# Kernel tuning notes

Measured on AMD Instinct MI355X. Metric: run time of the kernel, lower is better.

Reference implementation:

```python
import jax, jax.numpy as jnp
import numpy as np
import math

B, S, C = 4, 2048, 128
H, DK, DV, K = 8, 64, 64, 3


def setup_inputs() -> dict:
    key = jax.random.key(0)
    ks = jax.random.split(key, 12)
    sd = 0.05
    return {
        "x": jax.random.normal(ks[0], (B, S, C), dtype=jnp.float32),
        "length": jax.random.randint(ks[1], (B,), 1, S + 1, dtype=jnp.int32),
        "wq": jax.random.normal(ks[2], (H * DK, C, K), dtype=jnp.float32) * sd,
        "bq": jnp.zeros((H * DK,), dtype=jnp.float32),
        "wk": jax.random.normal(ks[3], (H * DK, C, K), dtype=jnp.float32) * sd,
        "bk": jnp.zeros((H * DK,), dtype=jnp.float32),
        "wv": jax.random.normal(ks[4], (H * DV, C), dtype=jnp.float32) * sd,
        "bv": jnp.zeros((H * DV,), dtype=jnp.float32),
        "w1": jax.random.normal(ks[5], (DV, H * DV), dtype=jnp.float32) * sd,
        "b1": jnp.zeros((DV,), dtype=jnp.float32),
        "w2": jax.random.normal(ks[6], (1, DV), dtype=jnp.float32) * sd,
        "b2": jnp.zeros((1,), dtype=jnp.float32),
    }


def _causal_conv(x, w, b):
    # x: (b,s,c), w: (o,c,k) torch Conv1d layout -> (b,s,o), causal (left) padding
    y = jax.lax.conv_general_dilated(
        x.transpose(0, 2, 1), w, window_strides=(1,), padding=[(K - 1, 0)],
        dimension_numbers=("NCH", "OIH", "NCH"))
    return y.transpose(0, 2, 1) + b


def _split_heads(x, d):
    b, s, _ = x.shape
    return x.reshape(b, s, H, d).transpose(0, 2, 1, 3)  # (b,h,s,d)


def reference(x, length, wq, bq, wk, bk, wv, bv, w1, b1, w2, b2):
    q = _split_heads(_causal_conv(x, wq, bq), DK)            # (b,h,s,dk)
    k = _split_heads(_causal_conv(x, wk, bk), DK)            # (b,h,s,dk)
    v = _split_heads(jax.nn.relu(x @ wv.T + bv), DV)         # (b,h,s,dv)

    attn = jnp.einsum("bhqd,bhkd->bhqk", q, k) / math.sqrt(DK)
    # future mask: additive -1e9 above the diagonal (matches triu * -1e9 + softmax)
    future = jnp.triu(jnp.ones((S, S), dtype=attn.dtype), k=1) * (-1e9)
    score = jax.nn.softmax(attn + future, axis=-1)
    # padding mask: zero query rows >= length[b]
    row_valid = (jnp.arange(S)[None, :] < length[:, None]).astype(score.dtype)
    score = score * row_valid[:, None, :, None]              # (b,h,s,s)

    out1 = jnp.einsum("bhqk,bhkd->bhqd", score, v)           # (b,h,s,dv)
    out2 = out1.transpose(0, 2, 1, 3).reshape(x.shape[0], S, H * DV)
    out3 = jax.nn.relu(out2 @ w1.T + b1) @ w2.T + b2         # (b,s,1)
    return out3, score
```

## Files before the change

kernel.cpp:

```cpp
#include <hip/hip_runtime.h>

#define S_ 2048
#define C_ 128
#define B_ 4
#define H_ 8
#define D_ 64

typedef __attribute__((ext_vector_type(8))) short bf16x8;
typedef __attribute__((ext_vector_type(4))) float f32x4;

__device__ inline unsigned short f2bf(float f) {
    union { float f; unsigned int u; } c; c.f = f;
    unsigned int u = c.u;
    unsigned int r = (u + 0x7FFFu + ((u >> 16) & 1u)) >> 16;
    return (unsigned short)r;
}
__device__ inline float bf2f(unsigned short s) {
    union { unsigned int u; float f; } c; c.u = ((unsigned int)s) << 16;
    return c.f;
}

__global__ __launch_bounds__(256) void prep_kernel(
    const float* __restrict__ x,
    const float* __restrict__ wq, const float* __restrict__ wk,
    const float* __restrict__ wv, const float* __restrict__ w1,
    unsigned short* __restrict__ xh,
    unsigned short* __restrict__ wPackQ, unsigned short* __restrict__ wPackK,
    unsigned short* __restrict__ wPackV, float* __restrict__ w1T)
{
    int idx = blockIdx.x * 256 + threadIdx.x;
    if (idx < 1048576) {
        xh[idx] = f2bf(x[idx]);
    } else if (idx < 1245184) {
        int i = idx - 1048576;
        int t = i >> 16, r = i & 65535;
        int o = r >> 7, c = r & 127;
        wPackQ[i] = f2bf(wq[o * 384 + c * 3 + t]);
    } else if (idx < 1441792) {
        int i = idx - 1245184;
        int t = i >> 16, r = i & 65535;
        int o = r >> 7, c = r & 127;
        wPackK[i] = f2bf(wk[o * 384 + c * 3 + t]);
    } else if (idx < 1507328) {
        int i = idx - 1441792;
        wPackV[i] = f2bf(wv[i]);
    } else if (idx < 1540096) {
        int i = idx - 1507328;
        int j = i >> 6, d = i & 63;
        w1T[i] = w1[d * 512 + j];
    }
}

__global__ __launch_bounds__(256) void qkv_kernel(
    const unsigned short* __restrict__ xh,
    const unsigned short* __restrict__ wPackQ, const unsigned short* __restrict__ wPackK,
    const unsigned short* __restrict__ wPackV,
    const float* __restrict__ bq, const float* __restrict__ bk,
    const float* __restrict__ bv,
    unsigned short* __restrict__ Qh, unsigned short* __restrict__ Kh,
    unsigned short* __restrict__ VhT)
{
    __shared__ __align__(16) short xs[130 * 136];
    __shared__ __align__(16) short ws[64 * 136];

    int s0 = blockIdx.x * 128;
    int h = blockIdx.y;
    int b = blockIdx.z;
    int bh = b * H_ + h;
    int tid = threadIdx.x;
    int w = tid >> 6;
    int lane = tid & 63;
    int col = lane & 15;
    int quad = lane >> 4;

    for (int i = tid; i < 2080; i += 256) {
        int row = i >> 4, c8 = (i & 15) << 3;
        int s = s0 - 2 + row;
        uint4 v = {0u, 0u, 0u, 0u};
        if (s >= 0) v = *(const uint4*)&xh[((long)b * S_ + s) * C_ + c8];
        *(uint4*)&xs[row * 136 + c8] = v;
    }

    for (int sec = 0; sec < 3; sec++) {
        const unsigned short* wsel = (sec == 0) ? wPackQ : (sec == 1) ? wPackK : wPackV;
        int tlo = (sec == 2) ? 2 : 0;

        f32x4 acc[2][4];
        #pragma unroll
        for (int rt = 0; rt < 2; rt++)
            #pragma unroll
            for (int nt = 0; nt < 4; nt++) acc[rt][nt] = (f32x4){0.f, 0.f, 0.f, 0.f};

        for (int t = tlo; t < 3; t++) {
            if (!(sec == 0 && t == 0)) __syncthreads();
            long wbase = (sec == 2) ? ((long)h * 8192)
                                    : ((long)t * 65536 + (long)h * 8192);
            for (int i = tid; i < 1024; i += 256) {
                int row = i >> 4, c8 = (i & 15) << 3;
                *(uint4*)&ws[row * 136 + c8] = *(const uint4*)&wsel[wbase + row * 128 + c8];
            }
            __syncthreads();

            #pragma unroll
            for (int kc = 0; kc < 4; kc++) {
                int ko = kc * 32 + quad * 8;
                bf16x8 a0 = *(const bf16x8*)&xs[(w * 32 + col + t) * 136 + ko];
                bf16x8 a1 = *(const bf16x8*)&xs[(w * 32 + 16 + col + t) * 136 + ko];
                #pragma unroll
                for (int nt = 0; nt < 4; nt++) {
                    bf16x8 bfr = *(const bf16x8*)&ws[(nt * 16 + col) * 136 + ko];
                    acc[0][nt] = __builtin_amdgcn_mfma_f32_16x16x32_bf16(a0, bfr, acc[0][nt], 0, 0, 0);
                    acc[1][nt] = __builtin_amdgcn_mfma_f32_16x16x32_bf16(a1, bfr, acc[1][nt], 0, 0, 0);
                }
            }
        }

        if (sec == 0) {
            #pragma unroll
            for (int nt = 0; nt < 4; nt++) {
                float bias = bq[h * 64 + nt * 16 + col];
                #pragma unroll
                for (int rt = 0; rt < 2; rt++)
                    #pragma unroll
                    for (int r = 0; r < 4; r++) {
                        int s = s0 + w * 32 + rt * 16 + quad * 4 + r;
                        Qh[((long)bh * S_ + s) * D_ + nt * 16 + col] =
                            f2bf((acc[rt][nt][r] + bias) * 0.18033688011112042f);
                    }
            }
        } else if (sec == 1) {
            #pragma unroll
            for (int nt = 0; nt < 4; nt++) {
                float bias = bk[h * 64 + nt * 16 + col];
                #pragma unroll
                for (int rt = 0; rt < 2; rt++)
                    #pragma unroll
                    for (int r = 0; r < 4; r++) {
                        int s = s0 + w * 32 + rt * 16 + quad * 4 + r;
                        Kh[((long)bh * S_ + s) * D_ + nt * 16 + col] =
                            f2bf(acc[rt][nt][r] + bias);
                    }
            }
        } else {
            __syncthreads();
            #pragma unroll
            for (int nt = 0; nt < 4; nt++) {
                float bias = bv[h * 64 + nt * 16 + col];
                #pragma unroll
                for (int rt = 0; rt < 2; rt++)
                    #pragma unroll
                    for (int r = 0; r < 4; r++) {
                        int sl = w * 32 + rt * 16 + quad * 4 + r;
                        ws[(nt * 16 + col) * 136 + sl] =
                            (short)f2bf(fmaxf(acc[rt][nt][r] + bias, 0.f));
                    }
            }
            __syncthreads();
            for (int i = tid; i < 1024; i += 256) {
                int row = i >> 4, c8 = (i & 15) << 3;
                *(uint4*)&VhT[((long)bh * D_ + row) * S_ + s0 + c8] =
                    *(const uint4*)&ws[row * 136 + c8];
            }
        }
    }
}

#define PST 78
__global__ __launch_bounds__(256) void attn_kernel(
    const unsigned short* __restrict__ Qh, const unsigned short* __restrict__ Kh,
    const unsigned short* __restrict__ VhT, const int* __restrict__ length,
    float* __restrict__ score, float* __restrict__ out2)
{
    __shared__ __align__(16) short Pfh[64 * PST];

    int idx = blockIdx.x;
    int xcd = idx & 7;
    int slot = idx >> 3;
    int t = slot >> 2;
    int qt = (t < 16) ? t : 47 - t;
    int bh = xcd * 4 + (slot & 3);
    int b = bh >> 3, h = bh & 7;
    int q0 = qt * 64;
    int tid = threadIdx.x;
    int w = tid >> 6;
    int lane = tid & 63;
    int col = lane & 15;
    int quad = lane >> 4;
    int len = length[b];

    const unsigned short* Qb = Qh + (long)bh * S_ * D_;
    const unsigned short* Kb = Kh + (long)bh * S_ * D_;
    const unsigned short* Vtb = VhT + (long)bh * D_ * S_;
    float* scb = score + (long)bh * S_ * S_;

    int arow = w * 16 + col;
    bf16x8 aq0 = *(const bf16x8*)&Qb[(q0 + arow) * D_ + quad * 8];
    bf16x8 aq1 = *(const bf16x8*)&Qb[(q0 + arow) * D_ + 32 + quad * 8];

    float lrun[4];
    #pragma unroll
    for (int r = 0; r < 4; r++) lrun[r] = 0.f;

    for (int kt = 0; kt <= qt; kt++) {
        bf16x8 kf0[4], kf1[4];
        #pragma unroll
        for (int n = 0; n < 4; n++) {
            const unsigned short* kp = &Kb[(kt * 64 + n * 16 + col) * D_ + quad * 8];
            kf0[n] = *(const bf16x8*)kp;
            kf1[n] = *(const bf16x8*)(kp + 32);
        }
        f32x4 acc[4];
        #pragma unroll
        for (int n = 0; n < 4; n++) acc[n] = (f32x4){0.f, 0.f, 0.f, 0.f};
        #pragma unroll
        for (int n = 0; n < 4; n++) {
            acc[n] = __builtin_amdgcn_mfma_f32_16x16x32_bf16(aq0, kf0[n], acc[n], 0, 0, 0);
            acc[n] = __builtin_amdgcn_mfma_f32_16x16x32_bf16(aq1, kf1[n], acc[n], 0, 0, 0);
        }
        if (kt == qt) {
            #pragma unroll
            for (int n = 0; n < 4; n++) {
                int kk = kt * 64 + n * 16 + col;
                #pragma unroll
                for (int r = 0; r < 4; r++) {
                    int q = q0 + w * 16 + quad * 4 + r;
                    if (kk > q) acc[n][r] = -1.0e30f;
                }
            }
        }
        #pragma unroll
        for (int r = 0; r < 4; r++) {
            lrun[r] += exp2f(acc[0][r]) + exp2f(acc[1][r]) +
                       exp2f(acc[2][r]) + exp2f(acc[3][r]);
        }
    }

    #pragma unroll
    for (int off = 1; off < 16; off <<= 1) {
        #pragma unroll
        for (int r = 0; r < 4; r++) lrun[r] += __shfl_xor(lrun[r], off, 64);
    }
    float linv[4];
    #pragma unroll
    for (int r = 0; r < 4; r++) linv[r] = 1.0f / lrun[r];

    f32x4 oacc[4];
    #pragma unroll
    for (int n = 0; n < 4; n++) oacc[n] = (f32x4){0.f, 0.f, 0.f, 0.f};

    int prow = w * 16 + quad * 4;
    for (int kt = 0; kt <= qt; kt++) {
        bf16x8 kf0[4], kf1[4], vf0[4], vf1[4];
        #pragma unroll
        for (int n = 0; n < 4; n++) {
            const unsigned short* kp = &Kb[(kt * 64 + n * 16 + col) * D_ + quad * 8];
            kf0[n] = *(const bf16x8*)kp;
            kf1[n] = *(const bf16x8*)(kp + 32);
        }
        #pragma unroll
        for (int n = 0; n < 4; n++) {
            const unsigned short* vp = &Vtb[(n * 16 + col) * S_ + kt * 64 + quad * 8];
            vf0[n] = *(const bf16x8*)vp;
            vf1[n] = *(const bf16x8*)(vp + 32);
        }

        f32x4 acc[4];
        #pragma unroll
        for (int n = 0; n < 4; n++) acc[n] = (f32x4){0.f, 0.f, 0.f, 0.f};
        #pragma unroll
        for (int n = 0; n < 4; n++) {
            acc[n] = __builtin_amdgcn_mfma_f32_16x16x32_bf16(aq0, kf0[n], acc[n], 0, 0, 0);
            acc[n] = __builtin_amdgcn_mfma_f32_16x16x32_bf16(aq1, kf1[n], acc[n], 0, 0, 0);
        }

        bool diag = (kt == qt);
        #pragma unroll
        for (int n = 0; n < 4; n++) {
            int kk = kt * 64 + n * 16 + col;
            float p[4];
            #pragma unroll
            for (int r = 0; r < 4; r++) {
                int q = q0 + prow + r;
                float pv = exp2f(acc[n][r]) * linv[r];
                if (q >= len || (diag && kk > q)) pv = 0.f;
                p[r] = pv;
                __builtin_nontemporal_store(pv, &scb[(long)q * S_ + kk]);
            }
            unsigned int pk01, pk23;
            asm("v_cvt_pk_bf16_f32 %0, %1, %2" : "=v"(pk01) : "v"(p[0]), "v"(p[1]));
            asm("v_cvt_pk_bf16_f32 %0, %1, %2" : "=v"(pk23) : "v"(p[2]), "v"(p[3]));
            int pcol = n * 16 + col;
            Pfh[prow * PST + pcol]       = (short)(pk01 & 0xFFFFu);
            Pfh[(prow + 1) * PST + pcol] = (short)(pk01 >> 16);
            Pfh[(prow + 2) * PST + pcol] = (short)(pk23 & 0xFFFFu);
            Pfh[(prow + 3) * PST + pcol] = (short)(pk23 >> 16);
        }

        bf16x8 pa0 = *(const bf16x8*)&Pfh[(w * 16 + col) * PST + quad * 8];
        bf16x8 pa1 = *(const bf16x8*)&Pfh[(w * 16 + col) * PST + 32 + quad * 8];
        #pragma unroll
        for (int n = 0; n < 4; n++) {
            oacc[n] = __builtin_amdgcn_mfma_f32_16x16x32_bf16(pa0, vf0[n], oacc[n], 0, 0, 0);
            oacc[n] = __builtin_amdgcn_mfma_f32_16x16x32_bf16(pa1, vf1[n], oacc[n], 0, 0, 0);
        }
    }

    #pragma unroll
    for (int n = 0; n < 4; n++) {
        #pragma unroll
        for (int r = 0; r < 4; r++) {
            int q = q0 + w * 16 + quad * 4 + r;
            out2[((long)(b * S_ + q)) * 512 + h * 64 + n * 16 + col] = oacc[n][r];
        }
    }

    f32x4 z = (f32x4){0.f, 0.f, 0.f, 0.f};
    for (int kt2 = qt + 1; kt2 < 32; kt2++) {
        #pragma unroll
        for (int it = 0; it < 4; it++) {
            int idx2 = tid + it * 256;
            int rr = idx2 >> 4, cc = idx2 & 15;
            __builtin_nontemporal_store(z,
                (f32x4*)&scb[(long)(q0 + rr) * S_ + kt2 * 64 + cc * 4]);
        }
    }
}

__global__ __launch_bounds__(256) void mlp_kernel(
    const float* __restrict__ out2, const float* __restrict__ w1T,
    const float* __restrict__ b1, const float* __restrict__ w2,
    const float* __restrict__ b2, float* __restrict__ out3)
{
    __shared__ float xr[2048];
    int sg0 = blockIdx.x * 4;
    int tid = threadIdx.x;
    for (int i = tid; i < 2048; i += 256) xr[i] = out2[(long)sg0 * 512 + i];
    __syncthreads();

    int sl = tid >> 6, d = tid & 63;
    float acc = 0.f;
    const float* xp = &xr[sl * 512];
    #pragma unroll 8
    for (int j = 0; j < 512; j++) acc += xp[j] * w1T[j * 64 + d];
    float hval = fmaxf(acc + b1[d], 0.f);
    float p = hval * w2[d];
    #pragma unroll
    for (int off = 32; off > 0; off >>= 1) p += __shfl_xor(p, off, 64);
    if (d == 0) out3[sg0 + sl] = p + b2[0];
}

extern "C" void kernel_launch(void* const* d_in, const int* in_sizes, int n_in,
                              void* d_out, int out_size, void* d_ws, size_t ws_size,
                              hipStream_t stream) {
    const float* x      = (const float*)d_in[0];
    const int*   length = (const int*)  d_in[1];
    const float* wq     = (const float*)d_in[2];
    const float* bq     = (const float*)d_in[3];
    const float* wk     = (const float*)d_in[4];
    const float* bk     = (const float*)d_in[5];
    const float* wv     = (const float*)d_in[6];
    const float* bv     = (const float*)d_in[7];
    const float* w1     = (const float*)d_in[8];
    const float* b1     = (const float*)d_in[9];
    const float* w2     = (const float*)d_in[10];
    const float* b2     = (const float*)d_in[11];

    float* out3  = (float*)d_out;
    float* score = (float*)d_out + 8192;

    float* ws  = (float*)d_ws;
    unsigned short* xh     = (unsigned short*)ws;  ws += 524288;
    unsigned short* wPackQ = (unsigned short*)ws;  ws += 98304;
    unsigned short* wPackK = (unsigned short*)ws;  ws += 98304;
    unsigned short* wPackV = (unsigned short*)ws;  ws += 32768;
    float* w1T = ws;  ws += 32768;
    unsigned short* Qh  = (unsigned short*)ws;  ws += 2097152;
    unsigned short* Kh  = (unsigned short*)ws;  ws += 2097152;
    unsigned short* VhT = (unsigned short*)ws;  ws += 2097152;
    float* o2  = ws;  ws += 4194304;

    hipLaunchKernelGGL(prep_kernel, dim3(6016), dim3(256), 0, stream,
                       x, wq, wk, wv, w1, xh, wPackQ, wPackK, wPackV, w1T);
    hipLaunchKernelGGL(qkv_kernel, dim3(16, 8, 4), dim3(256), 0, stream,
                       xh, wPackQ, wPackK, wPackV, bq, bk, bv, Qh, Kh, VhT);
    hipLaunchKernelGGL(attn_kernel, dim3(1024), dim3(256), 0, stream,
                       Qh, Kh, VhT, length, score, o2);
    hipLaunchKernelGGL(mlp_kernel, dim3(2048), dim3(256), 0, stream,
                       o2, w1T, b1, w2, b2, out3);
}
```

Baseline: 759.1 us.

## Stage K/V tiles through double-buffered LDS and vectorize score stores

The attention kernel now stages K (and, in the second pass, transposed V) tiles into double-buffered shared memory with coalesced 16-byte loads. The next tile's loads are issued before the current tile's MFMA work, replacing per-lane scattered global fragment loads. Score writes go from scalar per-element stores to row-contiguous float4 nontemporal stores read back from the bf16 P tile. Because of that readback, stored scores are now bf16-rounded, which may affect accuracy. The prep and MLP kernels are also vectorized with float4 conversion and a repacked w1 layout, at the cost of extra barriers per tile.

```diff
diff --git a/kernel.cpp b/kernel.cpp
--- a/kernel.cpp
+++ b/kernel.cpp
@@ -26,28 +26,31 @@
     const float* __restrict__ wv, const float* __restrict__ w1,
     unsigned short* __restrict__ xh,
     unsigned short* __restrict__ wPackQ, unsigned short* __restrict__ wPackK,
-    unsigned short* __restrict__ wPackV, float* __restrict__ w1T)
+    unsigned short* __restrict__ wPackV, float* __restrict__ w1T4)
 {
     int idx = blockIdx.x * 256 + threadIdx.x;
-    if (idx < 1048576) {
-        xh[idx] = f2bf(x[idx]);
-    } else if (idx < 1245184) {
-        int i = idx - 1048576;
+    if (idx < 262144) {
+        float4 v = *(const float4*)&x[idx * 4];
+        ushort4 o;
+        o.x = f2bf(v.x); o.y = f2bf(v.y); o.z = f2bf(v.z); o.w = f2bf(v.w);
+        *(ushort4*)&xh[idx * 4] = o;
+    } else if (idx < 458752) {
+        int i = idx - 262144;
         int t = i >> 16, r = i & 65535;
         int o = r >> 7, c = r & 127;
         wPackQ[i] = f2bf(wq[o * 384 + c * 3 + t]);
-    } else if (idx < 1441792) {
-        int i = idx - 1245184;
+    } else if (idx < 655360) {
+        int i = idx - 458752;
         int t = i >> 16, r = i & 65535;
         int o = r >> 7, c = r & 127;
         wPackK[i] = f2bf(wk[o * 384 + c * 3 + t]);
-    } else if (idx < 1507328) {
-        int i = idx - 1441792;
+    } else if (idx < 720896) {
+        int i = idx - 655360;
         wPackV[i] = f2bf(wv[i]);
-    } else if (idx < 1540096) {
-        int i = idx - 1507328;
-        int j = i >> 6, d = i & 63;
-        w1T[i] = w1[d * 512 + j];
+    } else if (idx < 753664) {
+        int i = idx - 720896;
+        int jj = i & 3, d = (i >> 2) & 63, jb = i >> 8;
+        w1T4[i] = w1[d * 512 + jb * 4 + jj];
     }
 }
 
@@ -171,6 +174,7 @@
     const unsigned short* __restrict__ VhT, const int* __restrict__ length,
     float* __restrict__ score, float* __restrict__ out2)
 {
+    __shared__ __align__(16) short Kbuf[2][2][64 * 72];
     __shared__ __align__(16) short Pfh[64 * PST];
 
     int idx = blockIdx.x;
@@ -193,6 +197,8 @@
     const unsigned short* Vtb = VhT + (long)bh * D_ * S_;
     float* scb = score + (long)bh * S_ * S_;
 
+    int srow_ = tid >> 2, sc16_ = (tid & 3) * 16;
+
     int arow = w * 16 + col;
     bf16x8 aq0 = *(const bf16x8*)&Qb[(q0 + arow) * D_ + quad * 8];
     bf16x8 aq1 = *(const bf16x8*)&Qb[(q0 + arow) * D_ + 32 + quad * 8];
@@ -201,21 +207,30 @@
     #pragma unroll
     for (int r = 0; r < 4; r++) lrun[r] = 0.f;
 
+    {
+        *(uint4*)&Kbuf[0][0][srow_ * 72 + sc16_]     = *(const uint4*)&Kb[srow_ * D_ + sc16_];
+        *(uint4*)&Kbuf[0][0][srow_ * 72 + sc16_ + 8] = *(const uint4*)&Kb[srow_ * D_ + sc16_ + 8];
+    }
+    __syncthreads();
+
     for (int kt = 0; kt <= qt; kt++) {
-        bf16x8 kf0[4], kf1[4];
+        int buf = kt & 1;
+        if (kt < qt) {
+            *(uint4*)&Kbuf[1 - buf][0][srow_ * 72 + sc16_] =
+                *(const uint4*)&Kb[((kt + 1) * 64 + srow_) * D_ + sc16_];
+            *(uint4*)&Kbuf[1 - buf][0][srow_ * 72 + sc16_ + 8] =
+                *(const uint4*)&Kb[((kt + 1) * 64 + srow_) * D_ + sc16_ + 8];
+        }
+
+        f32x4 acc[4];
+        #pragma unroll
+        for (int n = 0; n < 4; n++) acc[n] = (f32x4){0.f, 0.f, 0.f, 0.f};
         #pragma unroll
         for (int n = 0; n < 4; n++) {
-            const unsigned short* kp = &Kb[(kt * 64 + n * 16 + col) * D_ + quad * 8];
-            kf0[n] = *(const bf16x8*)kp;
-            kf1[n] = *(const bf16x8*)(kp + 32);
-        }
-        f32x4 acc[4];
-        #pragma unroll
-        for (int n = 0; n < 4; n++) acc[n] = (f32x4){0.f, 0.f, 0.f, 0.f};
-        #pragma unroll
-        for (int n = 0; n < 4; n++) {
-            acc[n] = __builtin_amdgcn_mfma_f32_16x16x32_bf16(aq0, kf0[n], acc[n], 0, 0, 0);
-            acc[n] = __builtin_amdgcn_mfma_f32_16x16x32_bf16(aq1, kf1[n], acc[n], 0, 0, 0);
+            bf16x8 b0 = *(const bf16x8*)&Kbuf[buf][0][(n * 16 + col) * 72 + quad * 8];
+            acc[n] = __builtin_amdgcn_mfma_f32_16x16x32_bf16(aq0, b0, acc[n], 0, 0, 0);
+            bf16x8 b1 = *(const bf16x8*)&Kbuf[buf][0][(n * 16 + col) * 72 + 32 + quad * 8];
+            acc[n] = __builtin_amdgcn_mfma_f32_16x16x32_bf16(aq1, b1, acc[n], 0, 0, 0);
         }
         if (kt == qt) {
             #pragma unroll
@@ -233,6 +248,7 @@
             lrun[r] += exp2f(acc[0][r]) + exp2f(acc[1][r]) +
                        exp2f(acc[2][r]) + exp2f(acc[3][r]);
         }
+        __syncthreads();
     }
 
     #pragma unroll
@@ -249,61 +265,83 @@
     for (int n = 0; n < 4; n++) oacc[n] = (f32x4){0.f, 0.f, 0.f, 0.f};
 
     int prow = w * 16 + quad * 4;
-    for (int kt = 0; kt <= qt; kt++) {
-        bf16x8 kf0[4], kf1[4], vf0[4], vf1[4];
-        #pragma unroll
-        for (int n = 0; n < 4; n++) {
-            const unsigned short* kp = &Kb[(kt * 64 + n * 16 + col) * D_ + quad * 8];
-            kf0[n] = *(const bf16x8*)kp;
-            kf1[n] = *(const bf16x8*)(kp + 32);
-        }
-        #pragma unroll
-        for (int n = 0; n < 4; n++) {
-            const unsigned short* vp = &Vtb[(n * 16 + col) * S_ + kt * 64 + quad * 8];
-            vf0[n] = *(const bf16x8*)vp;
-            vf1[n] = *(const bf16x8*)(vp + 32);
-        }
-
-        f32x4 acc[4];
-        #pragma unroll
-        for (int n = 0; n < 4; n++) acc[n] = (f32x4){0.f, 0.f, 0.f, 0.f};
-        #pragma unroll
-        for (int n = 0; n < 4; n++) {
-            acc[n] = __builtin_amdgcn_mfma_f32_16x16x32_bf16(aq0, kf0[n], acc[n], 0, 0, 0);
-            acc[n] = __builtin_amdgcn_mfma_f32_16x16x32_bf16(aq1, kf1[n], acc[n], 0, 0, 0);
-        }
-
-        bool diag = (kt == qt);
-        #pragma unroll
-        for (int n = 0; n < 4; n++) {
-            int kk = kt * 64 + n * 16 + col;
-            float p[4];
-            #pragma unroll
-            for (int r = 0; r < 4; r++) {
-                int q = q0 + prow + r;
-                float pv = exp2f(acc[n][r]) * linv[r];
-                if (q >= len || (diag && kk > q)) pv = 0.f;
-                p[r] = pv;
-                __builtin_nontemporal_store(pv, &scb[(long)q * S_ + kk]);
-            }
-            unsigned int pk01, pk23;
-            asm("v_cvt_pk_bf16_f32 %0, %1, %2" : "=v"(pk01) : "v"(p[0]), "v"(p[1]));
-            asm("v_cvt_pk_bf16_f32 %0, %1, %2" : "=v"(pk23) : "v"(p[2]), "v"(p[3]));
-            int pcol = n * 16 + col;
-            Pfh[prow * PST + pcol]       = (short)(pk01 & 0xFFFFu);
-            Pfh[(prow + 1) * PST + pcol] = (short)(pk01 >> 16);
-            Pfh[(prow + 2) * PST + pcol] = (short)(pk23 & 0xFFFFu);
-            Pfh[(prow + 3) * PST + pcol] = (short)(pk23 >> 16);
-        }
-
-        bf16x8 pa0 = *(const bf16x8*)&Pfh[(w * 16 + col) * PST + quad * 8];
-        bf16x8 pa1 = *(const bf16x8*)&Pfh[(w * 16 + col) * PST + 32 + quad * 8];
-        #pragma unroll
-        for (int n = 0; n < 4; n++) {
-            oacc[n] = __builtin_amdgcn_mfma_f32_16x16x32_bf16(pa0, vf0[n], oacc[n], 0, 0, 0);
-            oacc[n] = __builtin_amdgcn_mfma_f32_16x16x32_bf16(pa1, vf1[n], oacc[n], 0, 0, 0);
-        }
-    }
+    int rlo = lane >> 4;
+    int c4 = (lane & 15) * 4;
+
+#define STAGE2(HALF, KT) do { \
+    *(uint4*)&Kbuf[HALF][0][srow_ * 72 + sc16_] = \
+        *(const uint4*)&Kb[((KT) * 64 + srow_) * D_ + sc16_]; \
+    *(uint4*)&Kbuf[HALF][0][srow_ * 72 + sc16_ + 8] = \
+        *(const uint4*)&Kb[((KT) * 64 + srow_) * D_ + sc16_ + 8]; \
+    *(uint4*)&Kbuf[HALF][1][srow_ * 72 + sc16_] = \
+        *(const uint4*)&Vtb[srow_ * S_ + (KT) * 64 + sc16_]; \
+    *(uint4*)&Kbuf[HALF][1][srow_ * 72 + sc16_ + 8] = \
+        *(const uint4*)&Vtb[srow_ * S_ + (KT) * 64 + sc16_ + 8]; \
+} while (0)
+
+#define TILE2(HALF, KT) do { \
+    f32x4 acc[4]; \
+    _Pragma("unroll") \
+    for (int n = 0; n < 4; n++) acc[n] = (f32x4){0.f, 0.f, 0.f, 0.f}; \
+    _Pragma("unroll") \
+    for (int n = 0; n < 4; n++) { \
+        bf16x8 b0 = *(const bf16x8*)&Kbuf[HALF][0][(n * 16 + col) * 72 + quad * 8]; \
+        acc[n] = __builtin_amdgcn_mfma_f32_16x16x32_bf16(aq0, b0, acc[n], 0, 0, 0); \
+        bf16x8 b1 = *(const bf16x8*)&Kbuf[HALF][0][(n * 16 + col) * 72 + 32 + quad * 8]; \
+        acc[n] = __builtin_amdgcn_mfma_f32_16x16x32_bf16(aq1, b1, acc[n], 0, 0, 0); \
+    } \
+    bool diag = ((KT) == qt); \
+    _Pragma("unroll") \
+    for (int n = 0; n < 4; n++) { \
+        int kk = (KT) * 64 + n * 16 + col; \
+        _Pragma("unroll") \
+        for (int r = 0; r < 4; r++) { \
+            int q = q0 + prow + r; \
+            float pv = exp2f(acc[n][r]) * linv[r]; \
+            if (q >= len || (diag && kk > q)) pv = 0.f; \
+            Pfh[(prow + r) * PST + n * 16 + col] = (short)f2bf(pv); \
+        } \
+    } \
+    bf16x8 pa0 = *(const bf16x8*)&Pfh[(w * 16 + col) * PST + quad * 8]; \
+    bf16x8 pa1 = *(const bf16x8*)&Pfh[(w * 16 + col) * PST + 32 + quad * 8]; \
+    _Pragma("unroll") \
+    for (int n = 0; n < 4; n++) { \
+        bf16x8 vv0 = *(const bf16x8*)&Kbuf[HALF][1][(n * 16 + col) * 72 + quad * 8]; \
+        oacc[n] = __builtin_amdgcn_mfma_f32_16x16x32_bf16(pa0, vv0, oacc[n], 0, 0, 0); \
+        bf16x8 vv1 = *(const bf16x8*)&Kbuf[HALF][1][(n * 16 + col) * 72 + 32 + quad * 8]; \
+        oacc[n] = __builtin_amdgcn_mfma_f32_16x16x32_bf16(pa1, vv1, oacc[n], 0, 0, 0); \
+    } \
+    _Pragma("unroll") \
+    for (int j = 0; j < 4; j++) { \
+        int row = w * 16 + j * 4 + rlo; \
+        uint2 pk = *(const uint2*)&Pfh[row * PST + c4]; \
+        f32x4 v; \
+        v[0] = bf2f((unsigned short)(pk.x & 0xFFFFu)); \
+        v[1] = bf2f((unsigned short)(pk.x >> 16)); \
+        v[2] = bf2f((unsigned short)(pk.y & 0xFFFFu)); \
+        v[3] = bf2f((unsigned short)(pk.y >> 16)); \
+        __builtin_nontemporal_store(v, \
+            (f32x4*)&scb[(long)(q0 + row) * S_ + (KT) * 64 + c4]); \
+    } \
+} while (0)
+
+    STAGE2(0, 0);
+    __syncthreads();
+    {
+        int kt = 0;
+        while (true) {
+            if (kt < qt) STAGE2(1, kt + 1);
+            TILE2(0, kt);
+            __syncthreads();
+            kt++; if (kt > qt) break;
+            if (kt < qt) STAGE2(0, kt + 1);
+            TILE2(1, kt);
+            __syncthreads();
+            kt++; if (kt > qt) break;
+        }
+    }
+#undef STAGE2
+#undef TILE2
 
     #pragma unroll
     for (int n = 0; n < 4; n++) {
@@ -327,21 +365,25 @@
 }
 
 __global__ __launch_bounds__(256) void mlp_kernel(
-    const float* __restrict__ out2, const float* __restrict__ w1T,
+    const float* __restrict__ out2, const float* __restrict__ w1T4,
     const float* __restrict__ b1, const float* __restrict__ w2,
     const float* __restrict__ b2, float* __restrict__ out3)
 {
-    __shared__ float xr[2048];
+    __shared__ __align__(16) float xr[2048];
     int sg0 = blockIdx.x * 4;
     int tid = threadIdx.x;
-    for (int i = tid; i < 2048; i += 256) xr[i] = out2[(long)sg0 * 512 + i];
+    for (int i = tid; i < 512; i += 256)
+        *(f32x4*)&xr[i * 4] = *(const f32x4*)&out2[(long)sg0 * 512 + i * 4];
     __syncthreads();
 
     int sl = tid >> 6, d = tid & 63;
     float acc = 0.f;
-    const float* xp = &xr[sl * 512];
-    #pragma unroll 8
-    for (int j = 0; j < 512; j++) acc += xp[j] * w1T[j * 64 + d];
+    #pragma unroll 4
+    for (int jb = 0; jb < 128; jb++) {
+        f32x4 xv = *(const f32x4*)&xr[sl * 512 + jb * 4];
+        f32x4 wv = *(const f32x4*)&w1T4[jb * 256 + d * 4];
+        acc += xv[0] * wv[0] + xv[1] * wv[1] + xv[2] * wv[2] + xv[3] * wv[3];
+    }
     float hval = fmaxf(acc + b1[d], 0.f);
     float p = hval * w2[d];
     #pragma unroll
@@ -373,18 +415,18 @@
     unsigned short* wPackQ = (unsigned short*)ws;  ws += 98304;
     unsigned short* wPackK = (unsigned short*)ws;  ws += 98304;
     unsigned short* wPackV = (unsigned short*)ws;  ws += 32768;
-    float* w1T = ws;  ws += 32768;
+    float* w1T4 = ws;  ws += 32768;
     unsigned short* Qh  = (unsigned short*)ws;  ws += 2097152;
     unsigned short* Kh  = (unsigned short*)ws;  ws += 2097152;
     unsigned short* VhT = (unsigned short*)ws;  ws += 2097152;
     float* o2  = ws;  ws += 4194304;
 
-    hipLaunchKernelGGL(prep_kernel, dim3(6016), dim3(256), 0, stream,
-                       x, wq, wk, wv, w1, xh, wPackQ, wPackK, wPackV, w1T);
+    hipLaunchKernelGGL(prep_kernel, dim3(2944), dim3(256), 0, stream,
+                       x, wq, wk, wv, w1, xh, wPackQ, wPackK, wPackV, w1T4);
     hipLaunchKernelGGL(qkv_kernel, dim3(16, 8, 4), dim3(256), 0, stream,
                        xh, wPackQ, wPackK, wPackV, bq, bk, bv, Qh, Kh, VhT);
     hipLaunchKernelGGL(attn_kernel, dim3(1024), dim3(256), 0, stream,
                        Qh, Kh, VhT, length, score, o2);
     hipLaunchKernelGGL(mlp_kernel, dim3(2048), dim3(256), 0, stream,
-                       o2, w1T, b1, w2, b2, out3);
-}
+                       o2, w1T4, b1, w2, b2, out3);
+}
```

Measured after the change: 654.6 us. -13.8%, faster.
